# Optimization experiments

Hardware: AMD Instinct MI355X
Metric: run time of the kernel (lower is better)

The kernel has to match this reference:

```python
import jax, jax.numpy as jnp
import numpy as np

N_CAND = 10   # n_point_candidate
SIGMA = 1.0   # std threshold for vote filtering
EPS = 1e-6


def _get_pt_candidates(pcld, kpts_ofst, seg, cpt_ofst, k):
    # pcld [b,n,3]; kpts_ofst [b,n,8,3]; seg [b,n,1]; cpt_ofst [b,n,1,3]
    offsets = jnp.concatenate([kpts_ofst, cpt_ofst], axis=2)        # [b,n,9,3]
    scores = jnp.squeeze(seg, axis=-1)                              # [b,n]
    _, idx = jax.lax.top_k(scores, k)                               # [b,k] most confident points
    cands = pcld[:, :, None, :] + offsets                           # [b,n,9,3] candidate kpt positions
    cands = jnp.take_along_axis(cands, idx[:, :, None, None], axis=1)  # [b,k,9,3]
    return jnp.transpose(cands, (0, 2, 1, 3))                       # [b,9,k,3]


def _pts_clustering_with_std(kpts_cans, sigma=SIGMA):
    # kpts_cans [b,n_kpts,k,3]: keep candidates within sigma*std of the mean, average survivors
    mean = jnp.mean(kpts_cans, axis=2, keepdims=True)
    std = jnp.std(kpts_cans, axis=2, keepdims=True)
    inlier = jnp.all(jnp.abs(kpts_cans - mean) <= sigma * std, axis=-1)  # [b,n_kpts,k]
    w = inlier.astype(kpts_cans.dtype)[..., None]
    return jnp.sum(kpts_cans * w, axis=2) / (jnp.sum(w, axis=2) + EPS)   # [b,n_kpts,3]


def _rt_svd_transform(A, B, w):
    # Weighted Kabsch: find R,t with R @ A + t ~= B.  A,B [b,n,3]; w [n]
    wn = w / jnp.sum(w)
    cA = jnp.einsum('n,bnc->bc', wn, A)[:, None, :]                 # weighted centroids
    cB = jnp.einsum('n,bnc->bc', wn, B)[:, None, :]
    Am, Bm = A - cA, B - cB
    H = jnp.einsum('bni,n,bnj->bij', Am, w, Bm)                     # [b,3,3] cross-covariance
    U, S, Vh = jnp.linalg.svd(H)
    V = jnp.swapaxes(Vh, -1, -2)
    R0 = V @ jnp.swapaxes(U, -1, -2)
    flip = jnp.where(jnp.linalg.det(R0) < 0.0, -1.0, 1.0)           # reflection fix
    V = V.at[:, :, -1].multiply(flip[:, None])
    R = V @ jnp.swapaxes(U, -1, -2)                                 # [b,3,3]
    t = jnp.swapaxes(cB, -1, -2) - R @ jnp.swapaxes(cA, -1, -2)     # [b,3,1]
    return R, t


def setup_inputs() -> dict:
    key = jax.random.key(0)
    k1, k2, k3, k4, k5 = jax.random.split(key, 5)
    b, n, nk = 64, 12288, 8
    return {
        'pcld_input': jax.random.normal(k1, (b, n, 3), jnp.float32),
        'kpts_pre_input': jax.random.normal(k2, (b, n, nk, 3), jnp.float32),
        'cpt_pre_input': jax.random.normal(k3, (b, n, 1, 3), jnp.float32),
        'seg_pre_input': jax.random.uniform(k4, (b, n, 1), jnp.float32),
        'mesh_kpts_input': jax.random.normal(k5, (b, nk + 1, 3), jnp.float32),
    }


def reference(pcld_input, kpts_pre_input, cpt_pre_input, seg_pre_input, mesh_kpts_input):
    obj_kpts = _get_pt_candidates(pcld_input, kpts_pre_input, seg_pre_input, cpt_pre_input, N_CAND)
    kpts_voted = _pts_clustering_with_std(obj_kpts)                 # [b,9,3]
    n_pts = kpts_voted.shape[1]
    weights_vector = jnp.ones((n_pts,), dtype=kpts_voted.dtype)
    batch_R, batch_t = _rt_svd_transform(mesh_kpts_input, kpts_voted, weights_vector)
    batch_t = jnp.reshape(batch_t, (-1, 3))
    return batch_R, batch_t, kpts_voted
```

## Files before the change

### kernel.cpp

```cpp
#include <hip/hip_runtime.h>
#include <math.h>

typedef unsigned long long u64;
typedef unsigned int u32;

#define NB      64
#define NPTS    12288
#define KTOP    10
#define NKP     9
#define T       1024
#define CAND_MAX 128
#define THETA   0.997f

__device__ __forceinline__ u64 pack(float v, int idx) {
    return ((u64)__float_as_uint(v) << 32) | (u32)(~idx);
}
__device__ __forceinline__ int unpack_idx(u64 p) { return (int)(~(u32)p); }

__global__ __launch_bounds__(T)
void pose_fused(const float* __restrict__ pcld,
                const float* __restrict__ kpts,
                const float* __restrict__ cpt,
                const float* __restrict__ seg,
                const float* __restrict__ mesh,
                float* __restrict__ out)
{
    const int b = blockIdx.x;
    const int t = threadIdx.x;
    const int lane = t & 63;
    const int wid = t >> 6;

    __shared__ u64   cand[CAND_MAX];
    __shared__ int   cnt;
    __shared__ int   topidx[KTOP];
    __shared__ float cands[NKP][KTOP][3];
    __shared__ float voted[NKP][3];

    if (t == 0) cnt = 0;
    __syncthreads();

    const float4* segb4 = (const float4*)(seg + (size_t)b * NPTS);
    #pragma unroll
    for (int j = 0; j < 3; ++j) {
        int f4 = t + j * T;
        float4 a = segb4[f4];
        #pragma unroll
        for (int c = 0; c < 4; ++c) {
            float v = (c == 0) ? a.x : (c == 1) ? a.y : (c == 2) ? a.z : a.w;
            if (v >= THETA) {
                int slot = atomicAdd(&cnt, 1);
                if (slot < CAND_MAX) cand[slot] = pack(v, 4 * f4 + c);
            }
        }
    }
    __syncthreads();

    if (wid == 0) {
        int n = cnt;
        if (n >= KTOP && n <= CAND_MAX) {
            u64 a = (lane     < n) ? cand[lane]      : 0;
            u64 bq = (lane + 64 < n) ? cand[lane + 64] : 0;
            u64 hi = a > bq ? a : bq;
            u64 lo = a > bq ? bq : a;
            #pragma unroll
            for (int k = 0; k < KTOP; ++k) {
                u64 w = hi;
                #pragma unroll
                for (int s = 1; s < 64; s <<= 1) {
                    u64 o = __shfl_xor(w, s);
                    w = o > w ? o : w;
                }
                if (lane == 0) topidx[k] = unpack_idx(w);
                if (hi == w) { hi = lo; lo = 0; }
            }
        } else {
            const float* segb = seg + (size_t)b * NPTS;
            u64 loc[KTOP];
            #pragma unroll
            for (int j = 0; j < KTOP; ++j) loc[j] = 0;
            for (int i = lane; i < NPTS; i += 64) {
                u64 p = pack(segb[i], i);
                if (p > loc[KTOP - 1]) {
                    loc[KTOP - 1] = p;
                    #pragma unroll
                    for (int j = KTOP - 1; j > 0; --j) {
                        if (loc[j] > loc[j - 1]) { u64 tmp = loc[j]; loc[j] = loc[j - 1]; loc[j - 1] = tmp; }
                    }
                }
            }
            u64 cur = loc[0];
            #pragma unroll
            for (int k = 0; k < KTOP; ++k) {
                u64 w = cur;
                #pragma unroll
                for (int s = 1; s < 64; s <<= 1) {
                    u64 o = __shfl_xor(w, s);
                    w = o > w ? o : w;
                }
                if (lane == 0) topidx[k] = unpack_idx(w);
                if (cur == w) {
                    #pragma unroll
                    for (int i = 0; i + 1 < KTOP; ++i) loc[i] = loc[i + 1];
                    loc[KTOP - 1] = 0;
                    cur = loc[0];
                }
            }
        }
    }
    __syncthreads();

    if (t < NKP * KTOP) {
        int j = t / KTOP;
        int i = t % KTOP;
        int p = topidx[i];
        size_t base = (size_t)b * NPTS + p;
        float px = pcld[base * 3 + 0], py = pcld[base * 3 + 1], pz = pcld[base * 3 + 2];
        float ox, oy, oz;
        if (j < 8) {
            size_t kb = (base * 8 + j) * 3;
            ox = kpts[kb + 0]; oy = kpts[kb + 1]; oz = kpts[kb + 2];
        } else {
            size_t cb = base * 3;
            ox = cpt[cb + 0]; oy = cpt[cb + 1]; oz = cpt[cb + 2];
        }
        cands[j][i][0] = px + ox;
        cands[j][i][1] = py + oy;
        cands[j][i][2] = pz + oz;
    }
    __syncthreads();

    if (t < NKP) {
        float mean[3] = {0.f, 0.f, 0.f};
        for (int i = 0; i < KTOP; ++i)
            for (int c = 0; c < 3; ++c) mean[c] += cands[t][i][c];
        for (int c = 0; c < 3; ++c) mean[c] *= (1.0f / KTOP);
        float var[3] = {0.f, 0.f, 0.f};
        for (int i = 0; i < KTOP; ++i)
            for (int c = 0; c < 3; ++c) { float d = cands[t][i][c] - mean[c]; var[c] += d * d; }
        float sd[3];
        for (int c = 0; c < 3; ++c) sd[c] = sqrtf(var[c] * (1.0f / KTOP));
        float wsum = 0.f, acc[3] = {0.f, 0.f, 0.f};
        for (int i = 0; i < KTOP; ++i) {
            bool in = true;
            for (int c = 0; c < 3; ++c) in = in && (fabsf(cands[t][i][c] - mean[c]) <= sd[c]);
            if (in) {
                wsum += 1.f;
                for (int c = 0; c < 3; ++c) acc[c] += cands[t][i][c];
            }
        }
        float inv = 1.f / (wsum + 1e-6f);
        for (int c = 0; c < 3; ++c) {
            float v = acc[c] * inv;
            voted[t][c] = v;
            out[NB * 9 + NB * 3 + ((size_t)b * NKP + t) * 3 + c] = v;
        }
    }
    __syncthreads();

    if (t == 0) {
        const float* mb = mesh + (size_t)b * NKP * 3;
        float A[NKP][3], Bv[NKP][3];
        float cA[3] = {0, 0, 0}, cB[3] = {0, 0, 0};
        for (int n = 0; n < NKP; ++n) {
            for (int c = 0; c < 3; ++c) {
                A[n][c]  = mb[n * 3 + c];
                Bv[n][c] = voted[n][c];
                cA[c] += A[n][c];
                cB[c] += Bv[n][c];
            }
        }
        for (int c = 0; c < 3; ++c) { cA[c] *= (1.0f / NKP); cB[c] *= (1.0f / NKP); }

        float H[3][3] = {{0,0,0},{0,0,0},{0,0,0}};
        for (int n = 0; n < NKP; ++n)
            for (int i = 0; i < 3; ++i)
                for (int j = 0; j < 3; ++j)
                    H[i][j] += (A[n][i] - cA[i]) * (Bv[n][j] - cB[j]);

        float Km[3][3];
        for (int i = 0; i < 3; ++i)
            for (int j = 0; j < 3; ++j) {
                float s = 0;
                for (int l = 0; l < 3; ++l) s += H[l][i] * H[l][j];
                Km[i][j] = s;
            }

        float V[3][3] = {{1,0,0},{0,1,0},{0,0,1}};
        for (int sweep = 0; sweep < 5; ++sweep) {
            for (int p = 0; p < 2; ++p) {
                for (int q = p + 1; q < 3; ++q) {
                    float apq = Km[p][q];
                    float app = Km[p][p], aqq = Km[q][q];
                    if (fabsf(apq) <= 1e-12f * (fabsf(app) + fabsf(aqq)) || apq == 0.0f) continue;
                    float theta = (aqq - app) / (2.0f * apq);
                    float tj = ((theta >= 0.0f) ? 1.0f : -1.0f) / (fabsf(theta) + sqrtf(theta * theta + 1.0f));
                    float cj = 1.0f / sqrtf(tj * tj + 1.0f);
                    float sj = tj * cj;
                    for (int l = 0; l < 3; ++l) {
                        float klp = Km[l][p], klq = Km[l][q];
                        Km[l][p] = cj * klp - sj * klq;
                        Km[l][q] = sj * klp + cj * klq;
                    }
                    for (int l = 0; l < 3; ++l) {
                        float kpl = Km[p][l], kql = Km[q][l];
                        Km[p][l] = cj * kpl - sj * kql;
                        Km[q][l] = sj * kpl + cj * kql;
                    }
                    for (int l = 0; l < 3; ++l) {
                        float vlp = V[l][p], vlq = V[l][q];
                        V[l][p] = cj * vlp - sj * vlq;
                        V[l][q] = sj * vlp + cj * vlq;
                    }
                }
            }
        }

        float eig[3] = {Km[0][0], Km[1][1], Km[2][2]};
        int ord[3] = {0, 1, 2};
        if (eig[ord[0]] < eig[ord[1]]) { int tmp = ord[0]; ord[0] = ord[1]; ord[1] = tmp; }
        if (eig[ord[1]] < eig[ord[2]]) { int tmp = ord[1]; ord[1] = ord[2]; ord[2] = tmp; }
        if (eig[ord[0]] < eig[ord[1]]) { int tmp = ord[0]; ord[0] = ord[1]; ord[1] = tmp; }

        float detH =
            H[0][0] * (H[1][1] * H[2][2] - H[1][2] * H[2][1]) -
            H[0][1] * (H[1][0] * H[2][2] - H[1][2] * H[2][0]) +
            H[0][2] * (H[1][0] * H[2][1] - H[1][1] * H[2][0]);
        float dsign[3] = {1.0f, 1.0f, (detH < 0.0f) ? -1.0f : 1.0f};

        float R[3][3] = {{0,0,0},{0,0,0},{0,0,0}};
        for (int k = 0; k < 3; ++k) {
            int c = ord[k];
            float s = sqrtf(fmaxf(eig[c], 0.0f));
            float invs = 1.0f / fmaxf(s, 1e-12f);
            float u[3];
            for (int l = 0; l < 3; ++l) {
                float a = 0;
                for (int m = 0; m < 3; ++m) a += H[l][m] * V[m][c];
                u[l] = a * invs;
            }
            for (int r = 0; r < 3; ++r)
                for (int cc = 0; cc < 3; ++cc)
                    R[r][cc] += dsign[k] * V[r][c] * u[cc];
        }

        float tv[3];
        for (int c = 0; c < 3; ++c) {
            float a = 0;
            for (int m = 0; m < 3; ++m) a += R[c][m] * cA[m];
            tv[c] = cB[c] - a;
        }

        for (int r = 0; r < 3; ++r)
            for (int c = 0; c < 3; ++c)
                out[(size_t)b * 9 + r * 3 + c] = R[r][c];
        for (int c = 0; c < 3; ++c)
            out[NB * 9 + (size_t)b * 3 + c] = tv[c];
    }
}

extern "C" void kernel_launch(void* const* d_in, const int* in_sizes, int n_in,
                              void* d_out, int out_size, void* d_ws, size_t ws_size,
                              hipStream_t stream) {
    const float* pcld = (const float*)d_in[0];
    const float* kpts = (const float*)d_in[1];
    const float* cpt  = (const float*)d_in[2];
    const float* seg  = (const float*)d_in[3];
    const float* mesh = (const float*)d_in[4];
    float* out = (float*)d_out;

    pose_fused<<<NB, T, 0, stream>>>(pcld, kpts, cpt, seg, mesh, out);
}
```

Measured before the change: 125.4 us.

## Use rank-based top-k selection, prefetch mesh, float4 candidate storage, fast math intrinsics

Replaces the iterative shuffle-max top-k over the thresholded candidates with a rank count: each lane counts how many candidates beat its own and writes itself directly into its slot. The mesh keypoints are now loaded into shared memory early, overlapping with the seg scan. Candidates are stored as padded float4 in shared memory and unrolled into registers for the clustering step. The serial SVD code uses hardware rcp/rsq/sqrt intrinsics. Together these target the latency of the single-thread and single-wave tail stages, at a small cost in accuracy from the approximate math.

```diff
diff --git a/kernel.cpp b/kernel.cpp
--- a/kernel.cpp
+++ b/kernel.cpp
@@ -16,6 +16,10 @@
     return ((u64)__float_as_uint(v) << 32) | (u32)(~idx);
 }
 __device__ __forceinline__ int unpack_idx(u64 p) { return (int)(~(u32)p); }
+
+__device__ __forceinline__ float rcp_fast(float x)  { return __builtin_amdgcn_rcpf(x); }
+__device__ __forceinline__ float rsq_fast(float x)  { return __builtin_amdgcn_rsqf(x); }
+__device__ __forceinline__ float sqrt_fast(float x) { return __builtin_amdgcn_sqrtf(x); }
 
 __global__ __launch_bounds__(T)
 void pose_fused(const float* __restrict__ pcld,
@@ -30,13 +34,18 @@
     const int lane = t & 63;
     const int wid = t >> 6;
 
-    __shared__ u64   cand[CAND_MAX];
-    __shared__ int   cnt;
-    __shared__ int   topidx[KTOP];
-    __shared__ float cands[NKP][KTOP][3];
-    __shared__ float voted[NKP][3];
+    __shared__ u64    cand[CAND_MAX];
+    __shared__ int    cnt;
+    __shared__ int    topidx[KTOP];
+    __shared__ float4 cands4[NKP][KTOP];
+    __shared__ float  voted[NKP][3];
+    __shared__ float  meshS[NKP * 3];
 
     if (t == 0) cnt = 0;
+
+    float meshv = 0.0f;
+    if (t < NKP * 3) meshv = mesh[(size_t)b * (NKP * 3) + t];
+
     __syncthreads();
 
     const float4* segb4 = (const float4*)(seg + (size_t)b * NPTS);
@@ -53,26 +62,22 @@
             }
         }
     }
+    if (t < NKP * 3) meshS[t] = meshv;
     __syncthreads();
 
     if (wid == 0) {
         int n = cnt;
         if (n >= KTOP && n <= CAND_MAX) {
-            u64 a = (lane     < n) ? cand[lane]      : 0;
-            u64 bq = (lane + 64 < n) ? cand[lane + 64] : 0;
-            u64 hi = a > bq ? a : bq;
-            u64 lo = a > bq ? bq : a;
-            #pragma unroll
-            for (int k = 0; k < KTOP; ++k) {
-                u64 w = hi;
-                #pragma unroll
-                for (int s = 1; s < 64; s <<= 1) {
-                    u64 o = __shfl_xor(w, s);
-                    w = o > w ? o : w;
-                }
-                if (lane == 0) topidx[k] = unpack_idx(w);
-                if (hi == w) { hi = lo; lo = 0; }
-            }
+            u64 my0 = (lane < n)      ? cand[lane]      : 0;
+            u64 my1 = (lane + 64 < n) ? cand[lane + 64] : 0;
+            int r0 = 0, r1 = 0;
+            for (int i = 0; i < n; ++i) {
+                u64 ci = cand[i];
+                r0 += (ci > my0) ? 1 : 0;
+                r1 += (ci > my1) ? 1 : 0;
+            }
+            if (lane < n && r0 < KTOP)      topidx[r0] = unpack_idx(my0);
+            if (lane + 64 < n && r1 < KTOP) topidx[r1] = unpack_idx(my1);
         } else {
             const float* segb = seg + (size_t)b * NPTS;
             u64 loc[KTOP];
@@ -123,32 +128,47 @@
             size_t cb = base * 3;
             ox = cpt[cb + 0]; oy = cpt[cb + 1]; oz = cpt[cb + 2];
         }
-        cands[j][i][0] = px + ox;
-        cands[j][i][1] = py + oy;
-        cands[j][i][2] = pz + oz;
+        cands4[j][i] = make_float4(px + ox, py + oy, pz + oz, 0.0f);
     }
     __syncthreads();
 
     if (t < NKP) {
+        float4 c4[KTOP];
+        #pragma unroll
+        for (int i = 0; i < KTOP; ++i) c4[i] = cands4[t][i];
+
         float mean[3] = {0.f, 0.f, 0.f};
-        for (int i = 0; i < KTOP; ++i)
-            for (int c = 0; c < 3; ++c) mean[c] += cands[t][i][c];
+        #pragma unroll
+        for (int i = 0; i < KTOP; ++i) {
+            mean[0] += c4[i].x; mean[1] += c4[i].y; mean[2] += c4[i].z;
+        }
+        #pragma unroll
         for (int c = 0; c < 3; ++c) mean[c] *= (1.0f / KTOP);
+
         float var[3] = {0.f, 0.f, 0.f};
-        for (int i = 0; i < KTOP; ++i)
-            for (int c = 0; c < 3; ++c) { float d = cands[t][i][c] - mean[c]; var[c] += d * d; }
+        #pragma unroll
+        for (int i = 0; i < KTOP; ++i) {
+            float d0 = c4[i].x - mean[0]; var[0] += d0 * d0;
+            float d1 = c4[i].y - mean[1]; var[1] += d1 * d1;
+            float d2 = c4[i].z - mean[2]; var[2] += d2 * d2;
+        }
         float sd[3];
+        #pragma unroll
         for (int c = 0; c < 3; ++c) sd[c] = sqrtf(var[c] * (1.0f / KTOP));
+
         float wsum = 0.f, acc[3] = {0.f, 0.f, 0.f};
+        #pragma unroll
         for (int i = 0; i < KTOP; ++i) {
-            bool in = true;
-            for (int c = 0; c < 3; ++c) in = in && (fabsf(cands[t][i][c] - mean[c]) <= sd[c]);
+            bool in = (fabsf(c4[i].x - mean[0]) <= sd[0]) &&
+                      (fabsf(c4[i].y - mean[1]) <= sd[1]) &&
+                      (fabsf(c4[i].z - mean[2]) <= sd[2]);
             if (in) {
                 wsum += 1.f;
-                for (int c = 0; c < 3; ++c) acc[c] += cands[t][i][c];
+                acc[0] += c4[i].x; acc[1] += c4[i].y; acc[2] += c4[i].z;
             }
         }
         float inv = 1.f / (wsum + 1e-6f);
+        #pragma unroll
         for (int c = 0; c < 3; ++c) {
             float v = acc[c] * inv;
             voted[t][c] = v;
@@ -158,12 +178,11 @@
     __syncthreads();
 
     if (t == 0) {
-        const float* mb = mesh + (size_t)b * NKP * 3;
         float A[NKP][3], Bv[NKP][3];
         float cA[3] = {0, 0, 0}, cB[3] = {0, 0, 0};
         for (int n = 0; n < NKP; ++n) {
             for (int c = 0; c < 3; ++c) {
-                A[n][c]  = mb[n * 3 + c];
+                A[n][c]  = meshS[n * 3 + c];
                 Bv[n][c] = voted[n][c];
                 cA[c] += A[n][c];
                 cB[c] += Bv[n][c];
@@ -192,9 +211,10 @@
                     float apq = Km[p][q];
                     float app = Km[p][p], aqq = Km[q][q];
                     if (fabsf(apq) <= 1e-12f * (fabsf(app) + fabsf(aqq)) || apq == 0.0f) continue;
-                    float theta = (aqq - app) / (2.0f * apq);
-                    float tj = ((theta >= 0.0f) ? 1.0f : -1.0f) / (fabsf(theta) + sqrtf(theta * theta + 1.0f));
-                    float cj = 1.0f / sqrtf(tj * tj + 1.0f);
+                    float theta = (aqq - app) * rcp_fast(2.0f * apq);
+                    float tj = ((theta >= 0.0f) ? 1.0f : -1.0f) *
+                               rcp_fast(fabsf(theta) + sqrt_fast(theta * theta + 1.0f));
+                    float cj = rsq_fast(tj * tj + 1.0f);
                     float sj = tj * cj;
                     for (int l = 0; l < 3; ++l) {
                         float klp = Km[l][p], klq = Km[l][q];
@@ -230,8 +250,8 @@
         float R[3][3] = {{0,0,0},{0,0,0},{0,0,0}};
         for (int k = 0; k < 3; ++k) {
             int c = ord[k];
-            float s = sqrtf(fmaxf(eig[c], 0.0f));
-            float invs = 1.0f / fmaxf(s, 1e-12f);
+            float s = sqrt_fast(fmaxf(eig[c], 0.0f));
+            float invs = rcp_fast(fmaxf(s, 1e-12f));
             float u[3];
             for (int l = 0; l < 3; ++l) {
                 float a = 0;
```

Result: no change. 126.4 us (+0.8%).
